# Kernel optimization log

Measured on AMD Instinct MI355X. Metric: run time of the kernel, lower is better.

The kernel has to match this reference:

```python
import jax, jax.numpy as jnp
import numpy as np

B, S, D, H = 2, 2048, 1024, 16
DH = D // H  # dim per head (dim_singl_head)
SCALE = 0.02


def layer_norm(x, g, b, eps=1e-5):
    m = jnp.mean(x, axis=-1, keepdims=True)
    v = jnp.mean((x - m) ** 2, axis=-1, keepdims=True)
    return (x - m) / jnp.sqrt(v + eps) * g + b


def setup_inputs() -> dict:
    key = jax.random.key(0)
    ks = jax.random.split(key, 12)
    return {
        "query": jax.random.normal(ks[0], (B, S, D), jnp.float32),
        "key": jax.random.normal(ks[1], (B, S, D), jnp.float32),
        "value": jax.random.normal(ks[2], (B, S, D), jnp.float32),
        "mask": jax.random.randint(ks[3], (B, S), 0, 2).astype(jnp.int32),
        "Wq": jax.random.normal(ks[4], (D, D), jnp.float32) * SCALE,
        "bq": jnp.zeros((D,), jnp.float32),
        "Wk": jax.random.normal(ks[5], (D, D), jnp.float32) * SCALE,
        "bk": jnp.zeros((D,), jnp.float32),
        "Wv": jax.random.normal(ks[6], (D, D), jnp.float32) * SCALE,
        "bv": jnp.zeros((D,), jnp.float32),
        "g_att": jnp.ones((DH,), jnp.float32),
        "b_att": jnp.zeros((DH,), jnp.float32),
        "Wres": jax.random.normal(ks[7], (D, D), jnp.float32) * SCALE,
        "bres": jnp.zeros((D,), jnp.float32),
        "g_out": jnp.ones((D,), jnp.float32),
        "b_out": jnp.zeros((D,), jnp.float32),
    }


def reference(query, key, value, mask, Wq, bq, Wk, bk, Wv, bv,
              g_att, b_att, Wres, bres, g_out, b_out):
    # split heads: torch's split(dh,-1)+cat(dim=0) == [H,B,S,dh] layout
    def heads(x):
        return x.reshape(B, S, H, DH).transpose(2, 0, 1, 3)  # [H,B,S,dh]

    q = heads(query @ Wq + bq)
    k = heads(key @ Wk + bk)
    v = heads(value @ Wv + bv)

    # additive mask: (1-mask)*-1e9, broadcast [1,B,1,Sk]
    madd = (1.0 - mask.astype(q.dtype))[None, :, None, :] * -1e9

    scores = jnp.einsum('hbqd,hbkd->hbqk', q, k) / np.float32(np.sqrt(DH))
    w = jax.nn.softmax(scores + madd, axis=-1)
    out = jnp.einsum('hbqk,hbkd->hbqd', w, v)

    out = out + q                         # residual_att
    out = layer_norm(out, g_att, b_att)   # per-head LayerNorm on dh

    # concat heads back: [H,B,S,dh] -> [B,S,H*dh]
    out = out.transpose(1, 2, 0, 3).reshape(B, S, D)

    out = out + jnp.tanh(out @ Wres + bres)  # residual_out branch
    out = layer_norm(out, g_out, b_out)      # norm_out
    return jnp.tanh(out)                     # final activation
```

## Files before the change

kernel.cpp:

```cpp
#include <hip/hip_runtime.h>
#include <cstdint>
#include <cstddef>

#define BB 2
#define SS 2048
#define DD 1024
#define HH 16
#define DHH 64
#define MROWS (BB*SS)

typedef short short8 __attribute__((ext_vector_type(8)));
typedef short short4v __attribute__((ext_vector_type(4)));
typedef float floatx4 __attribute__((ext_vector_type(4)));

#define GAS __attribute__((address_space(1)))
#define LAS __attribute__((address_space(3)))

__device__ __forceinline__ float4 ld4(const float* p) { return *(const float4*)p; }

__device__ __forceinline__ short f2bf(float x) {
    unsigned u = __builtin_bit_cast(unsigned, x);
    unsigned r = (u + 0x7fffu + ((u >> 16) & 1u)) >> 16;
    return (short)r;
}

__device__ __forceinline__ void gl_lds16(const short* g, short* l) {
    __builtin_amdgcn_global_load_lds((const GAS unsigned int*)g,
                                     (LAS unsigned int*)l, 16, 0, 0);
}

__global__ __launch_bounds__(256) void convert_kernel(
    const float* __restrict__ s0, const float* __restrict__ s1, const float* __restrict__ s2,
    short* __restrict__ d0, short* __restrict__ d1, short* __restrict__ d2)
{
    const float* s; short* d;
    if (blockIdx.z == 0)      { s = s0; d = d0; }
    else if (blockIdx.z == 1) { s = s1; d = d1; }
    else                      { s = s2; d = d2; }
    size_t idx = ((size_t)blockIdx.x * 256 + threadIdx.x) * 8;
    float4 a = ld4(s + idx);
    float4 b = ld4(s + idx + 4);
    short8 p;
    p[0] = f2bf(a.x); p[1] = f2bf(a.y); p[2] = f2bf(a.z); p[3] = f2bf(a.w);
    p[4] = f2bf(b.x); p[5] = f2bf(b.y); p[6] = f2bf(b.z); p[7] = f2bf(b.w);
    *(short8*)(d + idx) = p;
}

__global__ __launch_bounds__(256) void transpose_w_kernel(
    const float* __restrict__ W0, const float* __restrict__ W1,
    const float* __restrict__ W2, const float* __restrict__ W3,
    short* __restrict__ T0, short* __restrict__ T1,
    short* __restrict__ T2, short* __restrict__ T3)
{
    const float* W; short* T;
    if (blockIdx.z == 0)      { W = W0; T = T0; }
    else if (blockIdx.z == 1) { W = W1; T = T1; }
    else if (blockIdx.z == 2) { W = W2; T = T2; }
    else                      { W = W3; T = T3; }

    __shared__ short tile[64 * 72];
    const int t  = threadIdx.x;
    const int k0 = blockIdx.x * 64, n0 = blockIdx.y * 64;
#pragma unroll
    for (int i = 0; i < 4; i++) {
        int flat = i * 256 + t;
        int row = flat >> 4;
        int c4  = (flat & 15) * 4;
        float4 v = ld4(W + (size_t)(k0 + row) * DD + n0 + c4);
        tile[(c4 + 0) * 72 + row] = f2bf(v.x);
        tile[(c4 + 1) * 72 + row] = f2bf(v.y);
        tile[(c4 + 2) * 72 + row] = f2bf(v.z);
        tile[(c4 + 3) * 72 + row] = f2bf(v.w);
    }
    __syncthreads();
#pragma unroll
    for (int i = 0; i < 4; i++) {
        int flat = i * 256 + t;
        int nrow = flat >> 4;
        int kc   = (flat & 15) * 4;
        short4v pk = *(short4v*)&tile[nrow * 72 + kc];
        *(short4v*)(T + (size_t)(n0 + nrow) * DD + k0 + kc) = pk;
    }
}

__global__ __launch_bounds__(256) void gemm_bf16_kernel(
    const short* __restrict__ A0, const short* __restrict__ A1, const short* __restrict__ A2,
    const short* __restrict__ Bt0, const short* __restrict__ Bt1, const short* __restrict__ Bt2,
    const float* __restrict__ b0, const float* __restrict__ b1, const float* __restrict__ b2,
    float* __restrict__ Cf0, float* __restrict__ Cf1, float* __restrict__ Cf2,
    short* __restrict__ Cb0, short* __restrict__ Cb1, short* __restrict__ Cb2,
    short* __restrict__ Ct0, short* __restrict__ Ct1, short* __restrict__ Ct2,
    float cs0, float cs1, float cs2)
{
    const short* A; const short* Bt; const float* bias;
    float* Cf; short* Cb; short* Ct; float cbs;
    if (blockIdx.z == 0)      { A = A0; Bt = Bt0; bias = b0; Cf = Cf0; Cb = Cb0; Ct = Ct0; cbs = cs0; }
    else if (blockIdx.z == 1) { A = A1; Bt = Bt1; bias = b1; Cf = Cf1; Cb = Cb1; Ct = Ct1; cbs = cs1; }
    else                      { A = A2; Bt = Bt2; bias = b2; Cf = Cf2; Cb = Cb2; Ct = Ct2; cbs = cs2; }

    __shared__ __align__(16) short As[128 * 32];
    __shared__ __align__(16) short Bs[128 * 32];

    const int tid  = threadIdx.x;
    const int lane = tid & 63;
    const int wave = tid >> 6;
    const int quad = lane >> 4;
    const int l15  = lane & 15;
    const int m0 = blockIdx.y * 128;
    const int n0 = blockIdx.x * 128;
    const int wr = (wave >> 1) * 64;
    const int wc = (wave & 1) * 64;

    floatx4 acc[4][4];
#pragma unroll
    for (int mt = 0; mt < 4; mt++)
#pragma unroll
        for (int nt = 0; nt < 4; nt++) acc[mt][nt] = (floatx4)0.0f;

    for (int k0 = 0; k0 < DD; k0 += 32) {
        __syncthreads();
#pragma unroll
        for (int j = 0; j < 2; j++) {
            int chunk = j * 256 + tid;
            int row = chunk >> 2;
            int ch  = chunk & 3;
            gl_lds16(A  + (size_t)(m0 + row) * DD + k0 + ch * 8, &As[chunk * 8]);
            gl_lds16(Bt + (size_t)(n0 + row) * DD + k0 + ch * 8, &Bs[chunk * 8]);
        }
        __syncthreads();

        short8 af[4], bf[4];
#pragma unroll
        for (int mt = 0; mt < 4; mt++)
            af[mt] = *(const short8*)&As[(wr + mt * 16 + l15) * 32 + quad * 8];
#pragma unroll
        for (int nt = 0; nt < 4; nt++)
            bf[nt] = *(const short8*)&Bs[(wc + nt * 16 + l15) * 32 + quad * 8];
#pragma unroll
        for (int mt = 0; mt < 4; mt++)
#pragma unroll
            for (int nt = 0; nt < 4; nt++)
                acc[mt][nt] = __builtin_amdgcn_mfma_f32_16x16x32_bf16(af[mt], bf[nt], acc[mt][nt], 0, 0, 0);
    }

    float biasv[4];
#pragma unroll
    for (int nt = 0; nt < 4; nt++) biasv[nt] = bias[n0 + wc + nt * 16 + l15];

    if (Cf || Cb) {
#pragma unroll
        for (int mt = 0; mt < 4; mt++)
#pragma unroll
            for (int r = 0; r < 4; r++) {
                const int m = m0 + wr + mt * 16 + quad * 4 + r;
                const size_t rowb = (size_t)m * DD + n0 + wc;
#pragma unroll
                for (int nt = 0; nt < 4; nt++) {
                    float v = acc[mt][nt][r] + biasv[nt];
                    if (Cf) Cf[rowb + nt * 16 + l15] = v;
                    if (Cb) Cb[rowb + nt * 16 + l15] = f2bf(v * cbs);
                }
            }
    }
    if (Ct) {
#pragma unroll
        for (int mt = 0; mt < 4; mt++) {
            const int mbase = m0 + wr + mt * 16 + quad * 4;
            const int bb = mbase >> 11;
            const int s0 = mbase & 2047;
#pragma unroll
            for (int nt = 0; nt < 4; nt++) {
                const int c = n0 + wc + nt * 16 + l15;
                short4v pk;
#pragma unroll
                for (int r = 0; r < 4; r++) pk[r] = f2bf(acc[mt][nt][r] + biasv[nt]);
                *(short4v*)(Ct + ((size_t)(bb * 1024 + c)) * SS + s0) = pk;
            }
        }
    }
}

__global__ __launch_bounds__(256, 2) void attn_mfma_kernel(
    const short* __restrict__ Qb, const short* __restrict__ Kb, const short* __restrict__ Vt,
    const float* __restrict__ Qf, const int* __restrict__ mask,
    const float* __restrict__ g_att, const float* __restrict__ b_att,
    float* __restrict__ X, short* __restrict__ Xb)
{
    const int tid  = threadIdx.x;
    const int lane = tid & 63;
    const int wave = tid >> 6;
    const int quad = lane >> 4;
    const int l15  = lane & 15;

    const int h  = blockIdx.y;
    const int b  = blockIdx.z;
    const int q0 = blockIdx.x * 128;
    const int bS = b * SS;

    __shared__ __align__(16) short Ks[2 * 64 * 72];
    __shared__ __align__(16) short Vs[2 * 64 * 72];
    __shared__ __align__(16) short Ps[4 * 32 * 68];
    __shared__ float smadd[2 * 64];

    short8 qf[2][2];
#pragma unroll
    for (int mt = 0; mt < 2; mt++)
#pragma unroll
        for (int s = 0; s < 2; s++)
            qf[mt][s] = *(const short8*)(Qb +
                (size_t)(bS + q0 + wave * 32 + mt * 16 + l15) * DD + h * 64 + s * 32 + quad * 8);

    floatx4 o[2][4];
#pragma unroll
    for (int mt = 0; mt < 2; mt++)
#pragma unroll
        for (int nt = 0; nt < 4; nt++) o[mt][nt] = (floatx4)0.0f;
    float lsum[2][4];
#pragma unroll
    for (int mt = 0; mt < 2; mt++)
#pragma unroll
        for (int r = 0; r < 4; r++) lsum[mt][r] = 0.0f;

    const int srow = tid >> 3;
    const int sch  = tid & 7;

    short8 kreg[2], vreg[2];
    float mreg;
    {
#pragma unroll
        for (int i = 0; i < 2; i++) {
            int row = srow + i * 32;
            kreg[i] = *(const short8*)(Kb + (size_t)(bS + row) * DD + h * 64 + sch * 8);
            vreg[i] = *(const short8*)(Vt + (size_t)(b * 1024 + h * 64 + row) * SS + sch * 8);
        }
        mreg = (tid < 64) ? (float)mask[bS + tid] : 0.0f;
    }

    for (int kt = 0; kt < SS / 64; kt++) {
        const int bufo = (kt & 1) * (64 * 72);
#pragma unroll
        for (int i = 0; i < 2; i++) {
            int row = srow + i * 32;
            *(short8*)&Ks[bufo + row * 72 + sch * 8] = kreg[i];
            *(short8*)&Vs[bufo + row * 72 + sch * 8] = vreg[i];
        }
        if (tid < 64) smadd[(kt & 1) * 64 + tid] = (1.0f - mreg) * -1e9f;

        if (kt < SS / 64 - 1) {
            const int k0n = (kt + 1) * 64;
#pragma unroll
            for (int i = 0; i < 2; i++) {
                int row = srow + i * 32;
                kreg[i] = *(const short8*)(Kb + (size_t)(bS + k0n + row) * DD + h * 64 + sch * 8);
                vreg[i] = *(const short8*)(Vt + (size_t)(b * 1024 + h * 64 + row) * SS + k0n + sch * 8);
            }
            mreg = (tid < 64) ? (float)mask[bS + k0n + tid] : 0.0f;
        }

        __builtin_amdgcn_s_waitcnt(0xC07F);
        __builtin_amdgcn_s_barrier();

        float mv[4];
#pragma unroll
        for (int nt = 0; nt < 4; nt++) mv[nt] = smadd[(kt & 1) * 64 + nt * 16 + l15];

#pragma unroll
        for (int mt = 0; mt < 2; mt++)
#pragma unroll
            for (int nt = 0; nt < 4; nt++) {
                floatx4 acc = (floatx4)0.0f;
#pragma unroll
                for (int s = 0; s < 2; s++) {
                    short8 bf = *(const short8*)&Ks[bufo + (nt * 16 + l15) * 72 + s * 32 + quad * 8];
                    acc = __builtin_amdgcn_mfma_f32_16x16x32_bf16(qf[mt][s], bf, acc, 0, 0, 0);
                }
#pragma unroll
                for (int r = 0; r < 4; r++) {
                    float p = __expf(acc[r] + mv[nt]);
                    lsum[mt][r] += p;
                    Ps[wave * 2176 + (mt * 16 + quad * 4 + r) * 68 + nt * 16 + l15] = f2bf(p);
                }
            }

#pragma unroll
        for (int s = 0; s < 2; s++) {
            short8 pa[2];
#pragma unroll
            for (int mt = 0; mt < 2; mt++)
                pa[mt] = *(const short8*)&Ps[wave * 2176 + (mt * 16 + l15) * 68 + s * 32 + quad * 8];
#pragma unroll
            for (int nt = 0; nt < 4; nt++) {
                short8 vb = *(const short8*)&Vs[bufo + (nt * 16 + l15) * 72 + s * 32 + quad * 8];
#pragma unroll
                for (int mt = 0; mt < 2; mt++)
                    o[mt][nt] = __builtin_amdgcn_mfma_f32_16x16x32_bf16(pa[mt], vb, o[mt][nt], 0, 0, 0);
            }
        }
    }

#pragma unroll
    for (int mt = 0; mt < 2; mt++)
#pragma unroll
        for (int r = 0; r < 4; r++)
#pragma unroll
            for (int off = 1; off < 16; off <<= 1)
                lsum[mt][r] += __shfl_xor(lsum[mt][r], off);

    float gvv[4], bvv[4];
#pragma unroll
    for (int nt = 0; nt < 4; nt++) { gvv[nt] = g_att[nt * 16 + l15]; bvv[nt] = b_att[nt * 16 + l15]; }

#pragma unroll
    for (int mt = 0; mt < 2; mt++) {
        float x[4][4];
        float sum[4] = {0.f, 0.f, 0.f, 0.f};
#pragma unroll
        for (int r = 0; r < 4; r++) {
            const float rl = 1.0f / lsum[mt][r];
            const int row = q0 + wave * 32 + mt * 16 + quad * 4 + r;
            const size_t base = (size_t)(bS + row) * DD + h * 64;
#pragma unroll
            for (int nt = 0; nt < 4; nt++) {
                float xv = o[mt][nt][r] * rl + Qf[base + nt * 16 + l15];
                x[nt][r] = xv;
                sum[r] += xv;
            }
        }
#pragma unroll
        for (int r = 0; r < 4; r++)
#pragma unroll
            for (int off = 1; off < 16; off <<= 1) sum[r] += __shfl_xor(sum[r], off);

        float vsum[4] = {0.f, 0.f, 0.f, 0.f}, mu[4];
#pragma unroll
        for (int r = 0; r < 4; r++) {
            mu[r] = sum[r] * (1.0f / 64.0f);
#pragma unroll
            for (int nt = 0; nt < 4; nt++) { float d = x[nt][r] - mu[r]; vsum[r] += d * d; }
        }
#pragma unroll
        for (int r = 0; r < 4; r++) {
#pragma unroll
            for (int off = 1; off < 16; off <<= 1) vsum[r] += __shfl_xor(vsum[r], off);
            float rstd = rsqrtf(vsum[r] * (1.0f / 64.0f) + 1e-5f);
            const int row = q0 + wave * 32 + mt * 16 + quad * 4 + r;
            const size_t base = (size_t)(bS + row) * DD + h * 64;
#pragma unroll
            for (int nt = 0; nt < 4; nt++) {
                float yv = (x[nt][r] - mu[r]) * rstd * gvv[nt] + bvv[nt];
                X[base + nt * 16 + l15] = yv;
                Xb[base + nt * 16 + l15] = f2bf(yv);
            }
        }
    }
}

__global__ __launch_bounds__(256) void lnout_kernel(
    const float* __restrict__ X, const float* __restrict__ Y,
    const float* __restrict__ g, const float* __restrict__ bcoef,
    float* __restrict__ out)
{
    const int r = blockIdx.x;
    const int t = threadIdx.x;
    const size_t base = (size_t)r * DD + (t << 2);
    float4 x = ld4(X + base);
    float4 y = ld4(Y + base);
    float4 z;
    z.x = x.x + tanhf(y.x);
    z.y = x.y + tanhf(y.y);
    z.z = x.z + tanhf(y.z);
    z.w = x.w + tanhf(y.w);

    __shared__ float red[4];
    __shared__ float stats[2];
    const int w = t >> 6;

    float sv = z.x + z.y + z.z + z.w;
#pragma unroll
    for (int off = 32; off > 0; off >>= 1) sv += __shfl_down(sv, off);
    if ((t & 63) == 0) red[w] = sv;
    __syncthreads();
    if (t == 0) stats[0] = (red[0] + red[1] + red[2] + red[3]) * (1.0f / 1024.0f);
    __syncthreads();
    const float mu = stats[0];

    float4 d;
    d.x = z.x - mu; d.y = z.y - mu; d.z = z.z - mu; d.w = z.w - mu;
    float s2 = d.x * d.x + d.y * d.y + d.z * d.z + d.w * d.w;
#pragma unroll
    for (int off = 32; off > 0; off >>= 1) s2 += __shfl_down(s2, off);
    if ((t & 63) == 0) red[w] = s2;
    __syncthreads();
    if (t == 0) stats[1] = rsqrtf((red[0] + red[1] + red[2] + red[3]) * (1.0f / 1024.0f) + 1e-5f);
    __syncthreads();
    const float rstd = stats[1];

    float4 gv = ld4(g + (t << 2));
    float4 bv = ld4(bcoef + (t << 2));
    float4 o;
    o.x = tanhf(d.x * rstd * gv.x + bv.x);
    o.y = tanhf(d.y * rstd * gv.y + bv.y);
    o.z = tanhf(d.z * rstd * gv.z + bv.z);
    o.w = tanhf(d.w * rstd * gv.w + bv.w);
    *(float4*)(out + base) = o;
}

extern "C" void kernel_launch(void* const* d_in, const int* in_sizes, int n_in,
                              void* d_out, int out_size, void* d_ws, size_t ws_size,
                              hipStream_t stream)
{
    const float* query = (const float*)d_in[0];
    const float* key   = (const float*)d_in[1];
    const float* value = (const float*)d_in[2];
    const int*   mask  = (const int*)  d_in[3];
    const float* Wq    = (const float*)d_in[4];
    const float* bq    = (const float*)d_in[5];
    const float* Wk    = (const float*)d_in[6];
    const float* bk    = (const float*)d_in[7];
    const float* Wv    = (const float*)d_in[8];
    const float* bv    = (const float*)d_in[9];
    const float* g_att = (const float*)d_in[10];
    const float* b_att = (const float*)d_in[11];
    const float* Wres  = (const float*)d_in[12];
    const float* bres  = (const float*)d_in[13];
    const float* g_out = (const float*)d_in[14];
    const float* b_out = (const float*)d_in[15];

    const size_t MAT = (size_t)MROWS * DD;
    float* fws = (float*)d_ws;
    float* Qw = fws;
    float* Xw = fws + MAT;
    short* Qb = (short*)(fws + 2 * MAT);
    short* Kb = Qb + MAT;
    short* Vt = Kb + MAT;
    short* qbf = Vt + MAT;
    short* kbf = qbf + MAT;
    short* vbf = kbf + MAT;
    short* Wtq = vbf + MAT;
    short* Wtk = Wtq + DD * DD;
    short* Wtv = Wtk + DD * DD;
    short* Wtr = Wtv + DD * DD;
    short* Xb = qbf;
    float* Yw = (float*)kbf;

    convert_kernel<<<dim3(MAT / 2048, 1, 3), 256, 0, stream>>>(
        query, key, value, qbf, kbf, vbf);

    transpose_w_kernel<<<dim3(16, 16, 4), 256, 0, stream>>>(
        Wq, Wk, Wv, Wres, Wtq, Wtk, Wtv, Wtr);

    gemm_bf16_kernel<<<dim3(8, 32, 3), 256, 0, stream>>>(
        qbf, kbf, vbf, Wtq, Wtk, Wtv, bq, bk, bv,
        Qw, nullptr, nullptr,
        Qb, Kb, nullptr,
        nullptr, nullptr, Vt,
        0.125f, 1.0f, 1.0f);

    attn_mfma_kernel<<<dim3(SS / 128, HH, BB), 256, 0, stream>>>(
        Qb, Kb, Vt, Qw, mask, g_att, b_att, Xw, Xb);

    gemm_bf16_kernel<<<dim3(8, 32, 1), 256, 0, stream>>>(
        Xb, Xb, Xb, Wtr, Wtr, Wtr, bres, bres, bres,
        Yw, Yw, Yw, nullptr, nullptr, nullptr, nullptr, nullptr, nullptr,
        1.0f, 1.0f, 1.0f);

    lnout_kernel<<<MROWS, 256, 0, stream>>>(Xw, Yw, g_out, b_out, (float*)d_out);
}
```

Baseline: 292.0 us.

## Transpose QK^T MFMA, use exp2 with prescaled Q, packed bf16 P stores

Swaps the MFMA operands so each lane holds four consecutive key columns of one query row. This makes the per-row sum a single scalar per lane, turns the mask load into a vector read, and lets P be stored as packed 8-byte bf16 writes via v_cvt_pk_bf16_f32. The Q scale folds in log2(e) so exp2 replaces expf. Row-sum reduction shrinks to two shuffles plus a broadcast. The cost is reduced P precision from hardware rounding, and correctness depends on the transposed accumulator layout mapping properly.

```diff
diff --git a/kernel.cpp b/kernel.cpp
--- a/kernel.cpp
+++ b/kernel.cpp
@@ -12,6 +12,7 @@
 typedef short short8 __attribute__((ext_vector_type(8)));
 typedef short short4v __attribute__((ext_vector_type(4)));
 typedef float floatx4 __attribute__((ext_vector_type(4)));
+typedef unsigned int uint2v __attribute__((ext_vector_type(2)));
 
 #define GAS __attribute__((address_space(1)))
 #define LAS __attribute__((address_space(3)))
@@ -22,6 +23,12 @@
     unsigned u = __builtin_bit_cast(unsigned, x);
     unsigned r = (u + 0x7fffu + ((u >> 16) & 1u)) >> 16;
     return (short)r;
+}
+
+__device__ __forceinline__ unsigned cvtpk(float lo, float hi) {
+    unsigned r;
+    asm("v_cvt_pk_bf16_f32 %0, %1, %2" : "=v"(r) : "v"(lo), "v"(hi));
+    return r;
 }
 
 __device__ __forceinline__ void gl_lds16(const short* g, short* l) {
@@ -215,11 +222,7 @@
     for (int mt = 0; mt < 2; mt++)
 #pragma unroll
         for (int nt = 0; nt < 4; nt++) o[mt][nt] = (floatx4)0.0f;
-    float lsum[2][4];
-#pragma unroll
-    for (int mt = 0; mt < 2; mt++)
-#pragma unroll
-        for (int r = 0; r < 4; r++) lsum[mt][r] = 0.0f;
+    float lsum[2] = {0.0f, 0.0f};
 
     const int srow = tid >> 3;
     const int sch  = tid & 7;
@@ -260,27 +263,28 @@
         __builtin_amdgcn_s_waitcnt(0xC07F);
         __builtin_amdgcn_s_barrier();
 
-        float mv[4];
-#pragma unroll
-        for (int nt = 0; nt < 4; nt++) mv[nt] = smadd[(kt & 1) * 64 + nt * 16 + l15];
-
-#pragma unroll
-        for (int mt = 0; mt < 2; mt++)
-#pragma unroll
-            for (int nt = 0; nt < 4; nt++) {
+#pragma unroll
+        for (int nt = 0; nt < 4; nt++) {
+            const float4 mrow = *(const float4*)&smadd[(kt & 1) * 64 + nt * 16 + quad * 4];
+#pragma unroll
+            for (int mt = 0; mt < 2; mt++) {
                 floatx4 acc = (floatx4)0.0f;
 #pragma unroll
                 for (int s = 0; s < 2; s++) {
-                    short8 bf = *(const short8*)&Ks[bufo + (nt * 16 + l15) * 72 + s * 32 + quad * 8];
-                    acc = __builtin_amdgcn_mfma_f32_16x16x32_bf16(qf[mt][s], bf, acc, 0, 0, 0);
+                    short8 kf = *(const short8*)&Ks[bufo + (nt * 16 + l15) * 72 + s * 32 + quad * 8];
+                    acc = __builtin_amdgcn_mfma_f32_16x16x32_bf16(kf, qf[mt][s], acc, 0, 0, 0);
                 }
-#pragma unroll
-                for (int r = 0; r < 4; r++) {
-                    float p = __expf(acc[r] + mv[nt]);
-                    lsum[mt][r] += p;
-                    Ps[wave * 2176 + (mt * 16 + quad * 4 + r) * 68 + nt * 16 + l15] = f2bf(p);
-                }
-            }
+                float p0 = __builtin_exp2f(acc[0] + mrow.x);
+                float p1 = __builtin_exp2f(acc[1] + mrow.y);
+                float p2 = __builtin_exp2f(acc[2] + mrow.z);
+                float p3 = __builtin_exp2f(acc[3] + mrow.w);
+                lsum[mt] += (p0 + p1) + (p2 + p3);
+                unsigned w0 = cvtpk(p0, p1);
+                unsigned w1 = cvtpk(p2, p3);
+                *(uint2v*)&Ps[wave * 2176 + (mt * 16 + l15) * 68 + nt * 16 + quad * 4]
+                    = (uint2v){w0, w1};
+            }
+        }
 
 #pragma unroll
         for (int s = 0; s < 2; s++) {
@@ -299,12 +303,16 @@
     }
 
 #pragma unroll
+    for (int mt = 0; mt < 2; mt++) {
+        lsum[mt] += __shfl_xor(lsum[mt], 16);
+        lsum[mt] += __shfl_xor(lsum[mt], 32);
+    }
+    float rlq[2][4];
+#pragma unroll
     for (int mt = 0; mt < 2; mt++)
 #pragma unroll
         for (int r = 0; r < 4; r++)
-#pragma unroll
-            for (int off = 1; off < 16; off <<= 1)
-                lsum[mt][r] += __shfl_xor(lsum[mt][r], off);
+            rlq[mt][r] = 1.0f / __shfl(lsum[mt], (lane & 48) | (quad * 4 + r));
 
     float gvv[4], bvv[4];
 #pragma unroll
@@ -316,7 +324,7 @@
         float sum[4] = {0.f, 0.f, 0.f, 0.f};
 #pragma unroll
         for (int r = 0; r < 4; r++) {
-            const float rl = 1.0f / lsum[mt][r];
+            const float rl = rlq[mt][r];
             const int row = q0 + wave * 32 + mt * 16 + quad * 4 + r;
             const size_t base = (size_t)(bS + row) * DD + h * 64;
 #pragma unroll
@@ -454,7 +462,7 @@
         Qw, nullptr, nullptr,
         Qb, Kb, nullptr,
         nullptr, nullptr, Vt,
-        0.125f, 1.0f, 1.0f);
+        0.180336884f, 1.0f, 1.0f);
 
     attn_mfma_kernel<<<dim3(SS / 128, HH, BB), 256, 0, stream>>>(
         Qb, Kb, Vt, Qw, mask, g_att, b_att, Xw, Xb);
```

After: 290.0 us. About the same (-0.7%).
